# Kernel optimization log

Hardware: AMD Instinct MI355X
Metric: run time of the kernel (lower is better)

Reference implementation:

```python
import jax, jax.numpy as jnp
import numpy as np

N = 100000
E = 1600000
IN_C = 128
HID = 32
HEADS = 4
OUT_C = 16
NEG_SLOPE = 0.2  # PyG GATConv default


def setup_inputs() -> dict:
    key = jax.random.key(0)
    ks = jax.random.split(key, 10)
    x = jax.random.normal(ks[0], (N, IN_C), dtype=jnp.float32)
    edge_index = jax.random.randint(ks[1], (2, E), 0, N, dtype=jnp.int64)
    # Layer 1 params (heads=4, concat=True)
    s1 = 1.0 / np.sqrt(IN_C)
    W1 = jax.random.normal(ks[2], (IN_C, HEADS * HID), dtype=jnp.float32) * s1
    a_src1 = jax.random.normal(ks[3], (HEADS, HID), dtype=jnp.float32) * s1
    a_dst1 = jax.random.normal(ks[4], (HEADS, HID), dtype=jnp.float32) * s1
    b1 = jnp.zeros((HEADS * HID,), dtype=jnp.float32)
    # Layer 2 params (heads=1, concat=False)
    s2 = 1.0 / np.sqrt(HEADS * HID)
    W2 = jax.random.normal(ks[5], (HEADS * HID, OUT_C), dtype=jnp.float32) * s2
    a_src2 = jax.random.normal(ks[6], (1, OUT_C), dtype=jnp.float32) * s2
    a_dst2 = jax.random.normal(ks[7], (1, OUT_C), dtype=jnp.float32) * s2
    b2 = jnp.zeros((OUT_C,), dtype=jnp.float32)
    return {"x": x, "edge_index": edge_index, "W1": W1, "a_src1": a_src1,
            "a_dst1": a_dst1, "b1": b1, "W2": W2, "a_src2": a_src2,
            "a_dst2": a_dst2, "b2": b2}


def _gat_layer(x, src, dst, W, a_src, a_dst, b, heads, out_c, concat):
    n = x.shape[0]
    h = (x @ W).reshape(n, heads, out_c)            # [N, H, C]
    al_s = jnp.sum(h * a_src, axis=-1)              # [N, H]
    al_d = jnp.sum(h * a_dst, axis=-1)              # [N, H]
    e = al_s[src] + al_d[dst]                       # [E, H]
    e = jnp.where(e > 0, e, NEG_SLOPE * e)          # LeakyReLU(0.2)
    # segment softmax over incoming edges per destination node
    m = jax.ops.segment_max(e, dst, num_segments=n)
    ex = jnp.exp(e - m[dst])
    denom = jax.ops.segment_sum(ex, dst, num_segments=n)
    alpha = ex / denom[dst]                         # [E, H]
    msg = h[src] * alpha[:, :, None]                # [E, H, C]
    out = jax.ops.segment_sum(msg, dst, num_segments=n)  # [N, H, C]
    out = out.reshape(n, heads * out_c) if concat else out.mean(axis=1)
    return out + b


def reference(x, edge_index, W1, a_src1, a_dst1, b1, W2, a_src2, a_dst2, b2):
    n = x.shape[0]
    loops = jnp.arange(n, dtype=edge_index.dtype)
    src = jnp.concatenate([edge_index[0], loops])   # PyG adds self-loops
    dst = jnp.concatenate([edge_index[1], loops])
    h = _gat_layer(x, src, dst, W1, a_src1, a_dst1, b1, HEADS, HID, True)
    h = jax.nn.relu(h)  # dropout is identity at inference
    out = _gat_layer(h, src, dst, W2, a_src2, a_dst2, b2, 1, OUT_C, False)
    return out
```

## Files before the change

kernel.cpp:

```cpp
#include <hip/hip_runtime.h>
#include <hip/hip_fp16.h>

#define N_NODES 100000
#define N_EDGES 1600000
#define E_TOT   (N_EDGES + N_NODES)
#define NEG_SLOPE 0.2f

#define BSH   9
#define BSZ   512
#define NBKT  ((N_NODES + BSZ - 1) / BSZ)
#define EPB   8192
#define PART_B ((E_TOT + EPB - 1) / EPB)

__device__ __forceinline__ float lrelu(float v) { return v > 0.f ? v : NEG_SLOPE * v; }

__device__ __forceinline__ float f16lo(unsigned u) {
    return __half2float(__ushort_as_half((unsigned short)(u & 0xFFFFu)));
}
__device__ __forceinline__ float f16hi(unsigned u) {
    return __half2float(__ushort_as_half((unsigned short)(u >> 16)));
}

__global__ __launch_bounds__(256) void k_bcount(const int* __restrict__ ei,
                                                int* __restrict__ bcnt) {
    __shared__ int lc[NBKT];
    int t = threadIdx.x;
    for (int i = t; i < NBKT; i += 256) lc[i] = 0;
    __syncthreads();
    size_t base = (size_t)blockIdx.x * EPB;
    for (int i = t; i < EPB; i += 256) {
        size_t e = base + i;
        if (e < E_TOT) {
            int d = (e < N_EDGES) ? ei[N_EDGES + e] : (int)(e - N_EDGES);
            atomicAdd(&lc[d >> BSH], 1);
        }
    }
    __syncthreads();
    for (int i = t; i < NBKT; i += 256) if (lc[i]) atomicAdd(&bcnt[i], lc[i]);
}

__global__ __launch_bounds__(256) void k_bscan(const int* __restrict__ bcnt,
                                               int* __restrict__ bbase,
                                               int* __restrict__ gcur,
                                               int* __restrict__ rowptr) {
    int t = threadIdx.x;
    int v = (t < NBKT) ? bcnt[t] : 0;
    __shared__ int ps[256];
    ps[t] = v;
    __syncthreads();
    for (int off = 1; off < 256; off <<= 1) {
        int u = (t >= off) ? ps[t - off] : 0;
        __syncthreads();
        ps[t] += u;
        __syncthreads();
    }
    int ex = ps[t] - v;
    if (t < NBKT) { bbase[t] = ex; gcur[t] = ex; }
    if (t == 0) { bbase[NBKT] = E_TOT; rowptr[N_NODES] = E_TOT; }
}

__global__ __launch_bounds__(256) void k_part(const int* __restrict__ ei,
                                              int* __restrict__ gcur,
                                              int* __restrict__ packed) {
    __shared__ int lcnt[NBKT];
    __shared__ int gpos[NBKT];
    __shared__ int lcur[NBKT];
    int t = threadIdx.x;
    for (int i = t; i < NBKT; i += 256) lcnt[i] = 0;
    __syncthreads();
    size_t base = (size_t)blockIdx.x * EPB;
    for (int i = t; i < EPB; i += 256) {
        size_t e = base + i;
        if (e < E_TOT) {
            int d = (e < N_EDGES) ? ei[N_EDGES + e] : (int)(e - N_EDGES);
            atomicAdd(&lcnt[d >> BSH], 1);
        }
    }
    __syncthreads();
    for (int i = t; i < NBKT; i += 256) {
        int c = lcnt[i];
        gpos[i] = c ? atomicAdd(&gcur[i], c) : 0;
        lcur[i] = 0;
    }
    __syncthreads();
    for (int i = t; i < EPB; i += 256) {
        size_t e = base + i;
        if (e < E_TOT) {
            int s, d;
            if (e < N_EDGES) { s = ei[e]; d = ei[N_EDGES + e]; }
            else             { s = (int)(e - N_EDGES); d = s; }
            int b = d >> BSH;
            int c = atomicAdd(&lcur[b], 1);
            packed[gpos[b] + c] = ((d & (BSZ - 1)) << 17) | s;
        }
    }
}

__global__ __launch_bounds__(512) void k_build(const int* __restrict__ packed,
                                               const int* __restrict__ bbase,
                                               int* __restrict__ rowptr,
                                               int* __restrict__ col) {
    int t = threadIdx.x;
    int b = blockIdx.x;
    int nb = b << BSH;
    __shared__ int cnt[BSZ];
    __shared__ int ps[BSZ];
    cnt[t] = 0;
    __syncthreads();
    int ebeg = bbase[b], eend = bbase[b + 1];
    for (int i = ebeg + t; i < eend; i += 512)
        atomicAdd(&cnt[packed[i] >> 17], 1);
    __syncthreads();
    int v = cnt[t];
    ps[t] = v;
    __syncthreads();
    for (int off = 1; off < 512; off <<= 1) {
        int u = (t >= off) ? ps[t - off] : 0;
        __syncthreads();
        ps[t] += u;
        __syncthreads();
    }
    int myofs = ebeg + ps[t] - v;
    int n = nb + t;
    if (n < N_NODES) rowptr[n] = myofs;
    __syncthreads();
    cnt[t] = myofs;
    __syncthreads();
    for (int i = ebeg + t; i < eend; i += 512) {
        int p = packed[i];
        int pos = atomicAdd(&cnt[p >> 17], 1);
        col[pos] = p & 0x1FFFF;
    }
}

__global__ __launch_bounds__(256) void k_gemm1(const float* __restrict__ x,
                                               const float* __restrict__ W1,
                                               const float* __restrict__ a_src,
                                               const float* __restrict__ a_dst,
                                               unsigned short* __restrict__ h1h,
                                               float* __restrict__ als,
                                               float* __restrict__ ald) {
    __shared__ float xs[64 * 128];
    int t = threadIdx.x;
    int c = t & 31, rg = t >> 5;
    int nb = blockIdx.x * 64;
    const float4* xv4 = (const float4*)x;
    float4* xs4 = (float4*)xs;
    size_t base4 = (size_t)nb * 32;
    const size_t lim4 = (size_t)N_NODES * 32;
#pragma unroll
    for (int i = 0; i < 8; ++i) {
        size_t g = base4 + t + i * 256;
        if (g < lim4) xs4[t + i * 256] = xv4[g];
    }
    __syncthreads();
    const float4* W1v = (const float4*)W1;
    float4 acc[8];
#pragma unroll
    for (int i = 0; i < 8; ++i) acc[i] = make_float4(0.f, 0.f, 0.f, 0.f);
#pragma unroll 4
    for (int k = 0; k < 128; ++k) {
        float4 w = W1v[k * 32 + c];
#pragma unroll
        for (int i = 0; i < 8; ++i) {
            float xv = xs[(rg + 8 * i) * 128 + k];
            acc[i].x = fmaf(xv, w.x, acc[i].x);
            acc[i].y = fmaf(xv, w.y, acc[i].y);
            acc[i].z = fmaf(xv, w.z, acc[i].z);
            acc[i].w = fmaf(xv, w.w, acc[i].w);
        }
    }
    float4 as4 = ((const float4*)a_src)[c];
    float4 ad4 = ((const float4*)a_dst)[c];
#pragma unroll
    for (int i = 0; i < 8; ++i) {
        int n = nb + rg + 8 * i;
        if (n < N_NODES) {
            ushort4 hb;
            hb.x = __half_as_ushort(__float2half(acc[i].x));
            hb.y = __half_as_ushort(__float2half(acc[i].y));
            hb.z = __half_as_ushort(__float2half(acc[i].z));
            hb.w = __half_as_ushort(__float2half(acc[i].w));
            ((ushort4*)h1h)[(size_t)n * 32 + c] = hb;
        }
        float vs = acc[i].x * as4.x + acc[i].y * as4.y + acc[i].z * as4.z + acc[i].w * as4.w;
        float vd = acc[i].x * ad4.x + acc[i].y * ad4.y + acc[i].z * ad4.z + acc[i].w * ad4.w;
        vs += __shfl_down(vs, 4, 8); vs += __shfl_down(vs, 2, 8); vs += __shfl_down(vs, 1, 8);
        vd += __shfl_down(vd, 4, 8); vd += __shfl_down(vd, 2, 8); vd += __shfl_down(vd, 1, 8);
        if ((c & 7) == 0 && n < N_NODES) {
            int h = c >> 3;
            als[n * 4 + h] = vs;
            ald[n * 4 + h] = vd;
        }
    }
}

__global__ __launch_bounds__(256) void k_agg1(const unsigned short* __restrict__ h1h,
                                              const float* __restrict__ als,
                                              const float* __restrict__ ald,
                                              const int* __restrict__ rowptr,
                                              const int* __restrict__ col,
                                              const float* __restrict__ b1,
                                              float* __restrict__ out1) {
    __shared__ float sex_all[4][64 * 4];
    __shared__ int   scol_all[4][64];
    int w = threadIdx.x >> 6;
    int lane = threadIdx.x & 63;
    int n = blockIdx.x * 4 + w;
    int slot = lane >> 4, cg = lane & 15;
    int hd = cg >> 2;
    float* sex = sex_all[w];
    int* scol = scol_all[w];
    float4 ald4 = ((const float4*)ald)[n];
    int beg = rowptr[n], end = rowptr[n + 1];
    float a0 = 0.f, a1 = 0.f, a2 = 0.f, a3 = 0.f;
    float a4 = 0.f, a5 = 0.f, a6 = 0.f, a7 = 0.f, den = 0.f;
    const float4* als4p = (const float4*)als;
    for (int base = beg; base < end; base += 64) {
        int cnt = min(64, end - base);
        int myc = 0;
        if (lane < cnt) myc = col[base + lane];
        __asm__ volatile("s_waitcnt lgkmcnt(0)" ::: "memory");
        if (lane < cnt) {
            scol[lane] = myc;
            float4 as4 = als4p[myc];
            float4 e4;
            e4.x = __expf(lrelu(as4.x + ald4.x));
            e4.y = __expf(lrelu(as4.y + ald4.y));
            e4.z = __expf(lrelu(as4.z + ald4.z));
            e4.w = __expf(lrelu(as4.w + ald4.w));
            ((float4*)sex)[lane] = e4;
        }
        __asm__ volatile("s_waitcnt lgkmcnt(0)" ::: "memory");
        for (int q4 = 0; q4 < cnt; q4 += 4) {
            int myq = q4 + slot;
            if (myq < cnt) {
                int s = scol[myq];
                float ex = sex[myq * 4 + hd];
                uint4 hv = *(const uint4*)((const char*)h1h + (((size_t)s << 8) + (cg << 4)));
                a0 = fmaf(ex, f16lo(hv.x), a0);
                a1 = fmaf(ex, f16hi(hv.x), a1);
                a2 = fmaf(ex, f16lo(hv.y), a2);
                a3 = fmaf(ex, f16hi(hv.y), a3);
                a4 = fmaf(ex, f16lo(hv.z), a4);
                a5 = fmaf(ex, f16hi(hv.z), a5);
                a6 = fmaf(ex, f16lo(hv.w), a6);
                a7 = fmaf(ex, f16hi(hv.w), a7);
                den += ex;
            }
        }
    }
    a0 += __shfl_xor(a0, 16, 64); a1 += __shfl_xor(a1, 16, 64);
    a2 += __shfl_xor(a2, 16, 64); a3 += __shfl_xor(a3, 16, 64);
    a4 += __shfl_xor(a4, 16, 64); a5 += __shfl_xor(a5, 16, 64);
    a6 += __shfl_xor(a6, 16, 64); a7 += __shfl_xor(a7, 16, 64);
    den += __shfl_xor(den, 16, 64);
    a0 += __shfl_xor(a0, 32, 64); a1 += __shfl_xor(a1, 32, 64);
    a2 += __shfl_xor(a2, 32, 64); a3 += __shfl_xor(a3, 32, 64);
    a4 += __shfl_xor(a4, 32, 64); a5 += __shfl_xor(a5, 32, 64);
    a6 += __shfl_xor(a6, 32, 64); a7 += __shfl_xor(a7, 32, 64);
    den += __shfl_xor(den, 32, 64);
    if (lane < 16) {
        float inv = 1.0f / den;
        float4 bA = ((const float4*)b1)[2 * lane];
        float4 bB = ((const float4*)b1)[2 * lane + 1];
        float4 oA, oB;
        oA.x = fmaxf(fmaf(a0, inv, bA.x), 0.f);
        oA.y = fmaxf(fmaf(a1, inv, bA.y), 0.f);
        oA.z = fmaxf(fmaf(a2, inv, bA.z), 0.f);
        oA.w = fmaxf(fmaf(a3, inv, bA.w), 0.f);
        oB.x = fmaxf(fmaf(a4, inv, bB.x), 0.f);
        oB.y = fmaxf(fmaf(a5, inv, bB.y), 0.f);
        oB.z = fmaxf(fmaf(a6, inv, bB.z), 0.f);
        oB.w = fmaxf(fmaf(a7, inv, bB.w), 0.f);
        ((float4*)out1)[(size_t)n * 32 + 2 * lane]     = oA;
        ((float4*)out1)[(size_t)n * 32 + 2 * lane + 1] = oB;
    }
}

__global__ __launch_bounds__(256) void k_gemm2(const float* __restrict__ out1,
                                               const float* __restrict__ W2,
                                               const float* __restrict__ a_src,
                                               const float* __restrict__ a_dst,
                                               float* __restrict__ h2,
                                               float* __restrict__ als,
                                               float* __restrict__ ald) {
    __shared__ float W2s[128 * 16];
    __shared__ float xs[16 * 132];
    int t = threadIdx.x;
#pragma unroll
    for (int i = 0; i < 8; ++i) W2s[t + i * 256] = W2[t + i * 256];
    size_t base = (size_t)blockIdx.x * 16 * 128;
#pragma unroll
    for (int i = 0; i < 8; ++i) {
        int idx = t + i * 256;
        xs[(idx >> 7) * 132 + (idx & 127)] = out1[base + idx];
    }
    __syncthreads();
    int r = t >> 4, c = t & 15;
    float acc = 0.f;
    const float* xr = &xs[r * 132];
#pragma unroll 8
    for (int k = 0; k < 128; ++k) acc = fmaf(xr[k], W2s[k * 16 + c], acc);
    int n = blockIdx.x * 16 + r;
    h2[(size_t)n * 16 + c] = acc;
    float vs = acc * a_src[c];
    float vd = acc * a_dst[c];
#pragma unroll
    for (int off = 8; off >= 1; off >>= 1) {
        vs += __shfl_down(vs, off, 16);
        vd += __shfl_down(vd, off, 16);
    }
    if (c == 0) { als[n] = vs; ald[n] = vd; }
}

__global__ __launch_bounds__(256) void k_agg2(const float* __restrict__ h2,
                                              const float* __restrict__ als,
                                              const float* __restrict__ ald,
                                              const int* __restrict__ rowptr,
                                              const int* __restrict__ col,
                                              const float* __restrict__ b2,
                                              float* __restrict__ out) {
    int wave = threadIdx.x >> 6;
    int lane = threadIdx.x & 63;
    int n = blockIdx.x * 4 + wave;
    int c = lane & 15, slot = lane >> 4;
    float ad = ald[n];
    int beg = rowptr[n], end = rowptr[n + 1];
    float acc = 0.f, den = 0.f;
    for (int idx = beg + slot; idx < end; idx += 4) {
        int s = col[idx];
        float ex = __expf(lrelu(als[s] + ad));
        acc = fmaf(ex, h2[(size_t)s * 16 + c], acc);
        den += ex;
    }
    acc += __shfl_xor(acc, 16, 64); den += __shfl_xor(den, 16, 64);
    acc += __shfl_xor(acc, 32, 64); den += __shfl_xor(den, 32, 64);
    if (slot == 0) out[(size_t)n * 16 + c] = acc / den + b2[c];
}

extern "C" void kernel_launch(void* const* d_in, const int* in_sizes, int n_in,
                              void* d_out, int out_size, void* d_ws, size_t ws_size,
                              hipStream_t stream) {
    const float* x   = (const float*)d_in[0];
    const int*   ei  = (const int*)d_in[1];
    const float* W1  = (const float*)d_in[2];
    const float* as1 = (const float*)d_in[3];
    const float* ad1 = (const float*)d_in[4];
    const float* b1  = (const float*)d_in[5];
    const float* W2  = (const float*)d_in[6];
    const float* as2 = (const float*)d_in[7];
    const float* ad2 = (const float*)d_in[8];
    const float* b2  = (const float*)d_in[9];
    float* out = (float*)d_out;

    char* ws = (char*)d_ws;
    size_t off = 0;
    auto alloc = [&](size_t bytes) -> void* {
        void* p = ws + off;
        off += (bytes + 255) & ~(size_t)255;
        return p;
    };
    unsigned short* h1h = (unsigned short*)alloc((size_t)N_NODES * 128 * 2);
    float* out1  = (float*)alloc((size_t)N_NODES * 128 * 4);
    float* als1v = (float*)alloc((size_t)N_NODES * 4 * 4);
    float* ald1v = (float*)alloc((size_t)N_NODES * 4 * 4);
    float* h2    = (float*)alloc((size_t)N_NODES * 16 * 4);
    float* als2v = (float*)alloc((size_t)N_NODES * 4);
    float* ald2v = (float*)alloc((size_t)N_NODES * 4);
    int* rowptr  = (int*)alloc((size_t)(N_NODES + 1) * 4);
    int* bcnt    = (int*)alloc((size_t)NBKT * 4);
    int* bbase   = (int*)alloc((size_t)(NBKT + 1) * 4);
    int* gcur    = (int*)alloc((size_t)NBKT * 4);
    int* packed  = (int*)alloc((size_t)E_TOT * 4);
    int* colA    = (int*)alloc((size_t)E_TOT * 4);

    hipMemsetAsync(bcnt, 0, (size_t)NBKT * 4, stream);

    k_bcount<<<PART_B, 256, 0, stream>>>(ei, bcnt);
    k_bscan<<<1, 256, 0, stream>>>(bcnt, bbase, gcur, rowptr);
    k_part<<<PART_B, 256, 0, stream>>>(ei, gcur, packed);
    k_build<<<NBKT, 512, 0, stream>>>(packed, bbase, rowptr, colA);
    k_gemm1<<<(N_NODES + 63) / 64, 256, 0, stream>>>(x, W1, as1, ad1, h1h, als1v, ald1v);
    k_agg1<<<N_NODES / 4, 256, 0, stream>>>(h1h, als1v, ald1v, rowptr, colA, b1, out1);
    k_gemm2<<<N_NODES / 16, 256, 0, stream>>>(out1, W2, as2, ad2, h2, als2v, ald2v);
    k_agg2<<<N_NODES / 4, 256, 0, stream>>>(h2, als2v, ald2v, rowptr, colA, b2, out);
}
```

Measured before the change: 363.4 us.

## Use fixed-capacity buckets, fp16 layer-2 features and restructured aggregation kernels

Replaces the bucket count and scan kernels with fixed-capacity per-bucket regions, so partitioning needs a single pass over the edges and per-node degrees are stored explicitly. Layer-2 features are stored in fp16, and the second aggregation stages edge indices and weights in shared memory, processing 16 edges per step with vector loads. The layer-1 aggregation inner loop becomes branchless with unrolling. The fixed capacity assumes no bucket exceeds 10240 edges, which holds for uniform random graphs but would overflow on skewed inputs.

```diff
diff --git a/kernel.cpp b/kernel.cpp
--- a/kernel.cpp
+++ b/kernel.cpp
@@ -9,6 +9,7 @@
 #define BSH   9
 #define BSZ   512
 #define NBKT  ((N_NODES + BSZ - 1) / BSZ)
+#define CAP   10240
 #define EPB   8192
 #define PART_B ((E_TOT + EPB - 1) / EPB)
 
@@ -21,42 +22,9 @@
     return __half2float(__ushort_as_half((unsigned short)(u >> 16)));
 }
 
-__global__ __launch_bounds__(256) void k_bcount(const int* __restrict__ ei,
-                                                int* __restrict__ bcnt) {
-    __shared__ int lc[NBKT];
-    int t = threadIdx.x;
-    for (int i = t; i < NBKT; i += 256) lc[i] = 0;
-    __syncthreads();
-    size_t base = (size_t)blockIdx.x * EPB;
-    for (int i = t; i < EPB; i += 256) {
-        size_t e = base + i;
-        if (e < E_TOT) {
-            int d = (e < N_EDGES) ? ei[N_EDGES + e] : (int)(e - N_EDGES);
-            atomicAdd(&lc[d >> BSH], 1);
-        }
-    }
-    __syncthreads();
-    for (int i = t; i < NBKT; i += 256) if (lc[i]) atomicAdd(&bcnt[i], lc[i]);
-}
-
-__global__ __launch_bounds__(256) void k_bscan(const int* __restrict__ bcnt,
-                                               int* __restrict__ bbase,
-                                               int* __restrict__ gcur,
-                                               int* __restrict__ rowptr) {
-    int t = threadIdx.x;
-    int v = (t < NBKT) ? bcnt[t] : 0;
-    __shared__ int ps[256];
-    ps[t] = v;
-    __syncthreads();
-    for (int off = 1; off < 256; off <<= 1) {
-        int u = (t >= off) ? ps[t - off] : 0;
-        __syncthreads();
-        ps[t] += u;
-        __syncthreads();
-    }
-    int ex = ps[t] - v;
-    if (t < NBKT) { bbase[t] = ex; gcur[t] = ex; }
-    if (t == 0) { bbase[NBKT] = E_TOT; rowptr[N_NODES] = E_TOT; }
+__global__ __launch_bounds__(256) void k_init(int* __restrict__ gcur) {
+    int t = threadIdx.x;
+    if (t < NBKT) gcur[t] = t * CAP;
 }
 
 __global__ __launch_bounds__(256) void k_part(const int* __restrict__ ei,
@@ -97,17 +65,19 @@
 }
 
 __global__ __launch_bounds__(512) void k_build(const int* __restrict__ packed,
-                                               const int* __restrict__ bbase,
+                                               const int* __restrict__ gcur,
                                                int* __restrict__ rowptr,
+                                               int* __restrict__ deg,
                                                int* __restrict__ col) {
     int t = threadIdx.x;
     int b = blockIdx.x;
     int nb = b << BSH;
+    int ebeg = b * CAP;
+    int eend = gcur[b];
     __shared__ int cnt[BSZ];
     __shared__ int ps[BSZ];
     cnt[t] = 0;
     __syncthreads();
-    int ebeg = bbase[b], eend = bbase[b + 1];
     for (int i = ebeg + t; i < eend; i += 512)
         atomicAdd(&cnt[packed[i] >> 17], 1);
     __syncthreads();
@@ -122,7 +92,7 @@
     }
     int myofs = ebeg + ps[t] - v;
     int n = nb + t;
-    if (n < N_NODES) rowptr[n] = myofs;
+    if (n < N_NODES) { rowptr[n] = myofs; deg[n] = v; }
     __syncthreads();
     cnt[t] = myofs;
     __syncthreads();
@@ -199,6 +169,7 @@
                                               const float* __restrict__ als,
                                               const float* __restrict__ ald,
                                               const int* __restrict__ rowptr,
+                                              const int* __restrict__ deg,
                                               const int* __restrict__ col,
                                               const float* __restrict__ b1,
                                               float* __restrict__ out1) {
@@ -212,14 +183,14 @@
     float* sex = sex_all[w];
     int* scol = scol_all[w];
     float4 ald4 = ((const float4*)ald)[n];
-    int beg = rowptr[n], end = rowptr[n + 1];
+    int beg = rowptr[n], dtot = deg[n];
     float a0 = 0.f, a1 = 0.f, a2 = 0.f, a3 = 0.f;
     float a4 = 0.f, a5 = 0.f, a6 = 0.f, a7 = 0.f, den = 0.f;
     const float4* als4p = (const float4*)als;
-    for (int base = beg; base < end; base += 64) {
-        int cnt = min(64, end - base);
+    for (int base = 0; base < dtot; base += 64) {
+        int cnt = min(64, dtot - base);
         int myc = 0;
-        if (lane < cnt) myc = col[base + lane];
+        if (lane < cnt) myc = col[beg + base + lane];
         __asm__ volatile("s_waitcnt lgkmcnt(0)" ::: "memory");
         if (lane < cnt) {
             scol[lane] = myc;
@@ -232,22 +203,22 @@
             ((float4*)sex)[lane] = e4;
         }
         __asm__ volatile("s_waitcnt lgkmcnt(0)" ::: "memory");
+#pragma unroll 2
         for (int q4 = 0; q4 < cnt; q4 += 4) {
             int myq = q4 + slot;
-            if (myq < cnt) {
-                int s = scol[myq];
-                float ex = sex[myq * 4 + hd];
-                uint4 hv = *(const uint4*)((const char*)h1h + (((size_t)s << 8) + (cg << 4)));
-                a0 = fmaf(ex, f16lo(hv.x), a0);
-                a1 = fmaf(ex, f16hi(hv.x), a1);
-                a2 = fmaf(ex, f16lo(hv.y), a2);
-                a3 = fmaf(ex, f16hi(hv.y), a3);
-                a4 = fmaf(ex, f16lo(hv.z), a4);
-                a5 = fmaf(ex, f16hi(hv.z), a5);
-                a6 = fmaf(ex, f16lo(hv.w), a6);
-                a7 = fmaf(ex, f16hi(hv.w), a7);
-                den += ex;
-            }
+            int cq = min(myq, cnt - 1);
+            int s = scol[cq];
+            float ex = (myq < cnt) ? sex[cq * 4 + hd] : 0.f;
+            uint4 hv = *(const uint4*)((const char*)h1h + (((size_t)s << 8) + (cg << 4)));
+            a0 = fmaf(ex, f16lo(hv.x), a0);
+            a1 = fmaf(ex, f16hi(hv.x), a1);
+            a2 = fmaf(ex, f16lo(hv.y), a2);
+            a3 = fmaf(ex, f16hi(hv.y), a3);
+            a4 = fmaf(ex, f16lo(hv.z), a4);
+            a5 = fmaf(ex, f16hi(hv.z), a5);
+            a6 = fmaf(ex, f16lo(hv.w), a6);
+            a7 = fmaf(ex, f16hi(hv.w), a7);
+            den += ex;
         }
     }
     a0 += __shfl_xor(a0, 16, 64); a1 += __shfl_xor(a1, 16, 64);
@@ -282,7 +253,7 @@
                                                const float* __restrict__ W2,
                                                const float* __restrict__ a_src,
                                                const float* __restrict__ a_dst,
-                                               float* __restrict__ h2,
+                                               unsigned short* __restrict__ h2h,
                                                float* __restrict__ als,
                                                float* __restrict__ ald) {
     __shared__ float W2s[128 * 16];
@@ -303,7 +274,7 @@
 #pragma unroll 8
     for (int k = 0; k < 128; ++k) acc = fmaf(xr[k], W2s[k * 16 + c], acc);
     int n = blockIdx.x * 16 + r;
-    h2[(size_t)n * 16 + c] = acc;
+    h2h[(size_t)n * 16 + c] = __half_as_ushort(__float2half(acc));
     float vs = acc * a_src[c];
     float vd = acc * a_dst[c];
 #pragma unroll
@@ -314,29 +285,67 @@
     if (c == 0) { als[n] = vs; ald[n] = vd; }
 }
 
-__global__ __launch_bounds__(256) void k_agg2(const float* __restrict__ h2,
+__global__ __launch_bounds__(256) void k_agg2(const unsigned short* __restrict__ h2h,
                                               const float* __restrict__ als,
                                               const float* __restrict__ ald,
                                               const int* __restrict__ rowptr,
+                                              const int* __restrict__ deg,
                                               const int* __restrict__ col,
                                               const float* __restrict__ b2,
                                               float* __restrict__ out) {
-    int wave = threadIdx.x >> 6;
+    __shared__ float sex_all[4][64];
+    __shared__ int   scol_all[4][64];
+    int w = threadIdx.x >> 6;
     int lane = threadIdx.x & 63;
-    int n = blockIdx.x * 4 + wave;
-    int c = lane & 15, slot = lane >> 4;
+    int n = blockIdx.x * 4 + w;
+    int slot = lane >> 2, q = lane & 3;
+    float* sex = sex_all[w];
+    int* scol = scol_all[w];
     float ad = ald[n];
-    int beg = rowptr[n], end = rowptr[n + 1];
-    float acc = 0.f, den = 0.f;
-    for (int idx = beg + slot; idx < end; idx += 4) {
-        int s = col[idx];
-        float ex = __expf(lrelu(als[s] + ad));
-        acc = fmaf(ex, h2[(size_t)s * 16 + c], acc);
-        den += ex;
-    }
-    acc += __shfl_xor(acc, 16, 64); den += __shfl_xor(den, 16, 64);
-    acc += __shfl_xor(acc, 32, 64); den += __shfl_xor(den, 32, 64);
-    if (slot == 0) out[(size_t)n * 16 + c] = acc / den + b2[c];
+    int beg = rowptr[n], dtot = deg[n];
+    float a0 = 0.f, a1 = 0.f, a2 = 0.f, a3 = 0.f, den = 0.f;
+    for (int base = 0; base < dtot; base += 64) {
+        int cnt = min(64, dtot - base);
+        int myc = 0;
+        if (lane < cnt) myc = col[beg + base + lane];
+        __asm__ volatile("s_waitcnt lgkmcnt(0)" ::: "memory");
+        if (lane < cnt) {
+            scol[lane] = myc;
+            sex[lane] = __expf(lrelu(als[myc] + ad));
+        }
+        __asm__ volatile("s_waitcnt lgkmcnt(0)" ::: "memory");
+#pragma unroll 2
+        for (int q16 = 0; q16 < cnt; q16 += 16) {
+            int myq = q16 + slot;
+            int cq = min(myq, cnt - 1);
+            int s = scol[cq];
+            float ex = (myq < cnt) ? sex[cq] : 0.f;
+            uint2 hv = *(const uint2*)((const char*)h2h + ((size_t)s * 32u + (q << 3)));
+            a0 = fmaf(ex, f16lo(hv.x), a0);
+            a1 = fmaf(ex, f16hi(hv.x), a1);
+            a2 = fmaf(ex, f16lo(hv.y), a2);
+            a3 = fmaf(ex, f16hi(hv.y), a3);
+            den += ex;
+        }
+    }
+#pragma unroll
+    for (int off = 4; off <= 32; off <<= 1) {
+        a0 += __shfl_xor(a0, off, 64);
+        a1 += __shfl_xor(a1, off, 64);
+        a2 += __shfl_xor(a2, off, 64);
+        a3 += __shfl_xor(a3, off, 64);
+        den += __shfl_xor(den, off, 64);
+    }
+    if (slot == 0) {
+        float inv = 1.0f / den;
+        float4 b4 = ((const float4*)b2)[q];
+        float4 o;
+        o.x = fmaf(a0, inv, b4.x);
+        o.y = fmaf(a1, inv, b4.y);
+        o.z = fmaf(a2, inv, b4.z);
+        o.w = fmaf(a3, inv, b4.w);
+        ((float4*)out)[(size_t)n * 4 + q] = o;
+    }
 }
 
 extern "C" void kernel_launch(void* const* d_in, const int* in_sizes, int n_in,
@@ -365,24 +374,20 @@
     float* out1  = (float*)alloc((size_t)N_NODES * 128 * 4);
     float* als1v = (float*)alloc((size_t)N_NODES * 4 * 4);
     float* ald1v = (float*)alloc((size_t)N_NODES * 4 * 4);
-    float* h2    = (float*)alloc((size_t)N_NODES * 16 * 4);
+    unsigned short* h2h = (unsigned short*)alloc((size_t)N_NODES * 16 * 2);
     float* als2v = (float*)alloc((size_t)N_NODES * 4);
     float* ald2v = (float*)alloc((size_t)N_NODES * 4);
-    int* rowptr  = (int*)alloc((size_t)(N_NODES + 1) * 4);
-    int* bcnt    = (int*)alloc((size_t)NBKT * 4);
-    int* bbase   = (int*)alloc((size_t)(NBKT + 1) * 4);
+    int* rowptr  = (int*)alloc((size_t)N_NODES * 4);
+    int* degv    = (int*)alloc((size_t)N_NODES * 4);
     int* gcur    = (int*)alloc((size_t)NBKT * 4);
-    int* packed  = (int*)alloc((size_t)E_TOT * 4);
-    int* colA    = (int*)alloc((size_t)E_TOT * 4);
-
-    hipMemsetAsync(bcnt, 0, (size_t)NBKT * 4, stream);
-
-    k_bcount<<<PART_B, 256, 0, stream>>>(ei, bcnt);
-    k_bscan<<<1, 256, 0, stream>>>(bcnt, bbase, gcur, rowptr);
+    int* packed  = (int*)alloc((size_t)NBKT * CAP * 4);
+    int* colA    = (int*)alloc((size_t)NBKT * CAP * 4);
+
+    k_init<<<1, 256, 0, stream>>>(gcur);
     k_part<<<PART_B, 256, 0, stream>>>(ei, gcur, packed);
-    k_build<<<NBKT, 512, 0, stream>>>(packed, bbase, rowptr, colA);
+    k_build<<<NBKT, 512, 0, stream>>>(packed, gcur, rowptr, degv, colA);
     k_gemm1<<<(N_NODES + 63) / 64, 256, 0, stream>>>(x, W1, as1, ad1, h1h, als1v, ald1v);
-    k_agg1<<<N_NODES / 4, 256, 0, stream>>>(h1h, als1v, ald1v, rowptr, colA, b1, out1);
-    k_gemm2<<<N_NODES / 16, 256, 0, stream>>>(out1, W2, as2, ad2, h2, als2v, ald2v);
-    k_agg2<<<N_NODES / 4, 256, 0, stream>>>(h2, als2v, ald2v, rowptr, colA, b2, out);
-}
+    k_agg1<<<N_NODES / 4, 256, 0, stream>>>(h1h, als1v, ald1v, rowptr, degv, colA, b1, out1);
+    k_gemm2<<<N_NODES / 16, 256, 0, stream>>>(out1, W2, as2, ad2, h2h, als2v, ald2v);
+    k_agg2<<<N_NODES / 4, 256, 0, stream>>>(h2h, als2v, ald2v, rowptr, degv, colA, b2, out);
+}
```

Result: faster. 331.7 us (-8.7%).
